# Kernel optimization log

Hardware: AMD Instinct MI355X
Metric: run time of the kernel (lower is better)

Reference implementation:

```python
import jax, jax.numpy as jnp
import numpy as np

B = 32          # num graphs
N = 4096        # nodes per graph (temporal length after reshape)
TOT = B * N     # 131072 total nodes
F = 64          # num_features
HS = 128        # hidden_dim_s
RS = 32         # rank_s
HT = 128        # hidden_dim_t
RT = 32         # rank_t
E = 1048576     # num edges


def setup_inputs() -> dict:
    key = jax.random.key(0)
    ks = jax.random.split(key, 20)
    x = jax.random.normal(ks[0], (TOT, F), jnp.float32)
    edge_index = jax.random.randint(ks[1], (2, E), 0, TOT, dtype=jnp.int64)
    batch = jnp.repeat(jnp.arange(B, dtype=jnp.int64), N)

    def lin(k, fan_in, fan_out):
        s = 1.0 / np.sqrt(fan_in)
        return jax.random.uniform(k, (fan_in, fan_out), jnp.float32, -s, s)

    def conv(k, cout, cin):
        s = 1.0 / np.sqrt(cin * 3)
        return jax.random.uniform(k, (cout, cin, 3), jnp.float32, -s, s)

    return {
        "x": x, "edge_index": edge_index, "batch": batch,
        "W1": lin(ks[2], F, HS), "b1": jnp.zeros((HS,), jnp.float32),
        "W2": lin(ks[3], HS, RS), "b2": jnp.zeros((RS,), jnp.float32),
        "W3": lin(ks[4], RS, HS), "b3": jnp.zeros((HS,), jnp.float32),
        "tW1": conv(ks[5], HT, HS), "tb1": jnp.zeros((HT,), jnp.float32),
        "tW2": conv(ks[6], RT, HT), "tb2": jnp.zeros((RT,), jnp.float32),
        "tW3": conv(ks[7], HT, RT), "tb3": jnp.zeros((HT,), jnp.float32),
        "Wpi": lin(ks[8], HT, 1), "bpi": jnp.zeros((1,), jnp.float32),
        "Wn": lin(ks[9], HT, 1), "bn": jnp.zeros((1,), jnp.float32),
        "Wp": lin(ks[10], HT, 1), "bp": jnp.zeros((1,), jnp.float32),
    }


def reference(x, edge_index, batch,
              W1, b1, W2, b2, W3, b3,
              tW1, tb1, tW2, tb2, tW3, tb3,
              Wpi, bpi, Wn, bn, Wp, bp):
    src, dst = edge_index[0], edge_index[1]
    n = x.shape[0]

    # GCN symmetric normalization with added self-loops (PyG GCNConv default)
    deg = jnp.zeros((n,), x.dtype).at[dst].add(1.0) + 1.0  # +1 self-loop
    dinv = jax.lax.rsqrt(deg)
    enorm = dinv[src] * dinv[dst]       # [E] edge normalization
    snorm = dinv * dinv                 # [n] self-loop normalization

    def gcn(h, W, b):
        h = h @ W                                            # [n, out]
        agg = jnp.zeros_like(h).at[dst].add(h[src] * enorm[:, None])
        return agg + h * snorm[:, None] + b

    xs = jax.nn.relu(gcn(x, W1, b1))
    xs = jax.nn.relu(gcn(xs, W2, b2))
    xs = jax.nn.relu(gcn(xs, W3, b3))    # [TOT, HS]

    num_graphs = B  # == batch.max() + 1 (batch is repeat(arange(B), N))
    xs = xs.reshape(num_graphs, -1, xs.shape[-1]).transpose(0, 2, 1)  # [B, HS, N]

    def conv1d(z, w, bias):
        y = jax.lax.conv_general_dilated(
            z, w, window_strides=(1,), padding=((1, 1),),
            dimension_numbers=("NCH", "OIH", "NCH"))
        return y + bias[None, :, None]

    xt = jax.nn.relu(conv1d(xs, tW1, tb1))
    xt = jax.nn.relu(conv1d(xt, tW2, tb2))
    xt = jax.nn.relu(conv1d(xt, tW3, tb3))                   # [B, HT, N]

    xt = xt.transpose(0, 2, 1).reshape(-1, xt.shape[1])      # [TOT, HT]

    pi = jax.nn.sigmoid(xt @ Wpi + bpi)
    nb = jax.nn.softplus(xt @ Wn + bn)
    p = jax.nn.sigmoid(xt @ Wp + bp)
    return (pi, nb, p)
```

## Files before the change

### kernel.cpp

```cpp
#include <hip/hip_runtime.h>
#include <cmath>

constexpr int TOT = 131072;
constexpr int NE  = 1048576;
constexpr int NMASK = 4095;

constexpr int NB   = 512;
constexpr int DPB  = 256;
constexpr int BCAP = 4096;
constexpr int EPB  = 8192;

typedef __attribute__((ext_vector_type(8))) short bf16x8;
typedef __attribute__((ext_vector_type(4))) float f32x4;

__device__ inline float bf2f(unsigned int u16) {
    union { unsigned int i; float f; } x; x.i = u16 << 16; return x.f;
}
__device__ inline unsigned short f2bf(float f) {
    union { float f; unsigned int i; } x; x.f = f;
    unsigned int r = (x.i + 0x7fffu + ((x.i >> 16) & 1u)) >> 16;
    return (unsigned short)r;
}
__device__ inline void unpack8(uint4 v, float* f) {
    f[0] = bf2f(v.x & 0xffffu); f[1] = bf2f(v.x >> 16);
    f[2] = bf2f(v.y & 0xffffu); f[3] = bf2f(v.y >> 16);
    f[4] = bf2f(v.z & 0xffffu); f[5] = bf2f(v.z >> 16);
    f[6] = bf2f(v.w & 0xffffu); f[7] = bf2f(v.w >> 16);
}
__device__ inline uint4 pack8(const float* f) {
    uint4 v;
    v.x = (unsigned)f2bf(f[0]) | ((unsigned)f2bf(f[1]) << 16);
    v.y = (unsigned)f2bf(f[2]) | ((unsigned)f2bf(f[3]) << 16);
    v.z = (unsigned)f2bf(f[4]) | ((unsigned)f2bf(f[5]) << 16);
    v.w = (unsigned)f2bf(f[6]) | ((unsigned)f2bf(f[7]) << 16);
    return v;
}

__global__ __launch_bounds__(256) void k_part(const int* __restrict__ src,
                                              const int* __restrict__ dst,
                                              int* __restrict__ gcur,
                                              unsigned* __restrict__ buf) {
    __shared__ int hist[NB];
    __shared__ int cbase[NB];
    __shared__ int lcur[NB];
    const int tid = threadIdx.x;
    const int e0 = blockIdx.x * EPB;

    for (int b = tid; b < NB; b += 256) hist[b] = 0;
    __syncthreads();
    for (int i = tid; i < EPB; i += 256)
        atomicAdd(&hist[dst[e0 + i] >> 8], 1);
    __syncthreads();
    for (int b = tid; b < NB; b += 256) {
        int c = hist[b];
        cbase[b] = (c > 0) ? atomicAdd(&gcur[b * 32], c) : 0;
        lcur[b] = 0;
    }
    __syncthreads();
    for (int i = tid; i < EPB; i += 256) {
        int e = e0 + i;
        int d = dst[e];
        int b = d >> 8;
        int p = atomicAdd(&lcur[b], 1);
        buf[b * BCAP + cbase[b] + p] = ((unsigned)src[e] << 8) | (unsigned)(d & 255);
    }
}

__global__ __launch_bounds__(256) void k_bcsr(const unsigned* __restrict__ buf,
                                              const int* __restrict__ gcur,
                                              int* __restrict__ adj,
                                              int2* __restrict__ rse,
                                              float* __restrict__ dinv) {
    __shared__ int cnt[DPB];
    __shared__ int start[DPB];
    __shared__ int cur[DPB];
    __shared__ int sc[DPB];
    const int b = blockIdx.x;
    const int tid = threadIdx.x;
    cnt[tid] = 0;
    __syncthreads();
    const int n = gcur[b * 32];
    const unsigned* eb = buf + b * BCAP;
    for (int i = tid; i < n; i += 256)
        atomicAdd(&cnt[eb[i] & 255u], 1);
    __syncthreads();
    int v = cnt[tid];
    sc[tid] = v;
    __syncthreads();
    for (int off = 1; off < 256; off <<= 1) {
        int a = sc[tid];
        int p = (tid >= off) ? sc[tid - off] : 0;
        __syncthreads();
        sc[tid] = a + p;
        __syncthreads();
    }
    int st = sc[tid] - v;
    start[tid] = st;
    cur[tid] = 0;
    int d = (b << 8) + tid;
    rse[d] = make_int2(b * BCAP + st, v);
    dinv[d] = rsqrtf((float)v + 1.0f);
    __syncthreads();
    for (int i = tid; i < n; i += 256) {
        unsigned w = eb[i];
        int dl = (int)(w & 255u);
        int p = atomicAdd(&cur[dl], 1);
        adj[b * BCAP + start[dl] + p] = (int)(w >> 8);
    }
}

__global__ __launch_bounds__(256) void k_packall(
    const float* __restrict__ W1, const float* __restrict__ W2, const float* __restrict__ W3,
    const float* __restrict__ tW1, const float* __restrict__ tW2, const float* __restrict__ tW3,
    unsigned short* __restrict__ g1, unsigned short* __restrict__ g2, unsigned short* __restrict__ g3,
    unsigned short* __restrict__ c1, unsigned short* __restrict__ c2, unsigned short* __restrict__ c3) {
    int gid = blockIdx.x * 256 + threadIdx.x;
    const float* w; unsigned short* wp; int CIN, COUT, taps, idx;
    if      (gid <  8192) { w = W1;  wp = g1; CIN = 64;  COUT = 128; taps = 1; idx = gid; }
    else if (gid < 12288) { w = W2;  wp = g2; CIN = 128; COUT = 32;  taps = 1; idx = gid - 8192; }
    else if (gid < 16384) { w = W3;  wp = g3; CIN = 32;  COUT = 128; taps = 1; idx = gid - 12288; }
    else if (gid < 65536) { w = tW1; wp = c1; CIN = 128; COUT = 128; taps = 3; idx = gid - 16384; }
    else if (gid < 77824) { w = tW2; wp = c2; CIN = 128; COUT = 32;  taps = 3; idx = gid - 65536; }
    else if (gid < 90112) { w = tW3; wp = c3; CIN = 32;  COUT = 128; taps = 3; idx = gid - 77824; }
    else return;
    int j = idx & 7;
    int L = (idx >> 3) & 63;
    int f = idx >> 9;
    int NT = COUT >> 4;
    int kc = f / NT, nt = f - kc * NT;
    int k = kc * 32 + (L >> 4) * 8 + j;
    int n = nt * 16 + (L & 15);
    float v;
    if (taps == 1) v = w[k * COUT + n];
    else { int t = k / CIN, c = k - t * CIN; v = w[(n * CIN + c) * 3 + t]; }
    wp[idx] = f2bf(v);
}

__global__ __launch_bounds__(256) void k_scale64b(const float4* __restrict__ x,
                                                  const float* __restrict__ dinv,
                                                  uint4* __restrict__ out) {
    int t = blockIdx.x * 256 + threadIdx.x;
    int row = t >> 3;
    float d = dinv[row];
    float4 v0 = x[t * 2], v1 = x[t * 2 + 1];
    float f[8] = { v0.x * d, v0.y * d, v0.z * d, v0.w * d,
                   v1.x * d, v1.y * d, v1.z * d, v1.w * d };
    out[t] = pack8(f);
}

template<int LC, int EPI>
__global__ __launch_bounds__(256) void k_gcsr(const uint4* __restrict__ xs,
                                              const int* __restrict__ adj,
                                              const int2* __restrict__ rse,
                                              const float* __restrict__ dinv,
                                              const float* __restrict__ bias,
                                              uint4* __restrict__ out) {
    int t = blockIdx.x * 256 + threadIdx.x;
    int d = t >> LC;
    int g = t & ((1 << LC) - 1);
    float a[8];
    unpack8(xs[t], a);
    int2 se = rse[d];
    int e = se.x, end = se.x + se.y;
    for (; e + 4 <= end; e += 4) {
        int s0 = adj[e], s1 = adj[e + 1], s2 = adj[e + 2], s3 = adj[e + 3];
        uint4 v0 = xs[(s0 << LC) + g];
        uint4 v1 = xs[(s1 << LC) + g];
        uint4 v2 = xs[(s2 << LC) + g];
        uint4 v3 = xs[(s3 << LC) + g];
        float f[8];
        unpack8(v0, f);
#pragma unroll
        for (int j = 0; j < 8; ++j) a[j] += f[j];
        unpack8(v1, f);
#pragma unroll
        for (int j = 0; j < 8; ++j) a[j] += f[j];
        unpack8(v2, f);
#pragma unroll
        for (int j = 0; j < 8; ++j) a[j] += f[j];
        unpack8(v3, f);
#pragma unroll
        for (int j = 0; j < 8; ++j) a[j] += f[j];
    }
    for (; e < end; ++e) {
        float f[8];
        unpack8(xs[(adj[e] << LC) + g], f);
#pragma unroll
        for (int j = 0; j < 8; ++j) a[j] += f[j];
    }
    float dv = dinv[d];
    if (EPI == 1) {
#pragma unroll
        for (int j = 0; j < 8; ++j)
            a[j] = fmaxf(fmaf(a[j], dv, bias[g * 8 + j]), 0.0f) * dv;
    } else {
#pragma unroll
        for (int j = 0; j < 8; ++j) a[j] *= dv;
    }
    out[t] = pack8(a);
}

template<int CIN, int COUT, int TAPS, bool RELU, bool BIAS, bool SOUT>
__global__ __launch_bounds__(256) void k_mm(const unsigned short* __restrict__ x,
                                            const bf16x8* __restrict__ wp,
                                            const float* __restrict__ bias,
                                            const float* __restrict__ dinv,
                                            unsigned short* __restrict__ y) {
    constexpr int ROWS = 64;
    constexpr int HALO = (TAPS == 3) ? 1 : 0;
    constexpr int TR = ROWS + 2 * HALO;
    constexpr int SC = CIN + 8;
    constexpr int NCH = CIN / 32;
    constexpr int NK = TAPS * NCH;
    constexpr int NT = COUT / 16;
    constexpr int WN = (COUT == 128) ? 2 : 1;
    constexpr int WM = (COUT == 128) ? 4 : 2;
    __shared__ __attribute__((aligned(16))) unsigned short tile[TR * SC];

    const int R0 = blockIdx.x * ROWS;
    const int n0 = R0 & NMASK; (void)n0;

    constexpr int NLD = TR * (CIN / 8);
    for (int idx = threadIdx.x; idx < NLD; idx += 256) {
        int tr = idx / (CIN / 8);
        int c8 = idx - tr * (CIN / 8);
        int ro = tr - HALO;
        bool valid = true;
        if (TAPS == 3) {
            if (ro < 0) valid = (n0 > 0);
            else if (ro >= ROWS) valid = (n0 + ROWS < 4096);
        }
        uint4 v = make_uint4(0, 0, 0, 0);
        if (valid) v = *(const uint4*)(x + (long)(R0 + ro) * CIN + c8 * 8);
        *(uint4*)(tile + tr * SC + c8 * 8) = v;
    }
    __syncthreads();

    const int lane = threadIdx.x & 63;
    const int w = threadIdx.x >> 6;
    const int l16 = lane & 15;
    const int q = lane >> 4;
    const int colbase = (COUT == 128) ? w * 32 : (w & 1) * 16;
    const int rowbase = (COUT == 128) ? 0 : (w >> 1) * 32;
    const int nt0 = colbase >> 4;

    f32x4 acc[WM][WN];
#pragma unroll
    for (int wm = 0; wm < WM; ++wm)
#pragma unroll
        for (int nt = 0; nt < WN; ++nt) acc[wm][nt] = (f32x4){0.f, 0.f, 0.f, 0.f};

    const bf16x8* __restrict__ wpl = wp + lane;

#pragma unroll
    for (int kc = 0; kc < NK; ++kc) {
        const int tap = (TAPS == 3) ? (kc / NCH) : 0;
        const int ch  = (TAPS == 3) ? (kc - tap * NCH) : kc;
        bf16x8 a[WM];
#pragma unroll
        for (int wm = 0; wm < WM; ++wm)
            a[wm] = *(const bf16x8*)(tile + (rowbase + wm * 16 + l16 + tap) * SC + ch * 32 + q * 8);
        bf16x8 b[WN];
#pragma unroll
        for (int nt = 0; nt < WN; ++nt)
            b[nt] = wpl[(kc * NT + nt0 + nt) * 64];
#pragma unroll
        for (int wm = 0; wm < WM; ++wm)
#pragma unroll
            for (int nt = 0; nt < WN; ++nt)
                acc[wm][nt] = __builtin_amdgcn_mfma_f32_16x16x32_bf16(a[wm], b[nt], acc[wm][nt], 0, 0, 0);
    }

#pragma unroll
    for (int wm = 0; wm < WM; ++wm) {
#pragma unroll
        for (int nt = 0; nt < WN; ++nt) {
            int col = colbase + nt * 16 + l16;
            float bi = BIAS ? bias[col] : 0.0f;
#pragma unroll
            for (int r = 0; r < 4; ++r) {
                int row = R0 + rowbase + wm * 16 + q * 4 + r;
                float v = acc[wm][nt][r] + bi;
                if (RELU) v = fmaxf(v, 0.0f);
                if (SOUT) v *= dinv[row];
                y[(long)row * COUT + col] = f2bf(v);
            }
        }
    }
}

__global__ __launch_bounds__(256) void k_conv_heads(
    const unsigned short* __restrict__ x, const bf16x8* __restrict__ wp,
    const float* __restrict__ bias,
    const float* __restrict__ Wpi, const float* __restrict__ bpi,
    const float* __restrict__ Wn,  const float* __restrict__ bn,
    const float* __restrict__ Wp,  const float* __restrict__ bp,
    float* __restrict__ out) {
    constexpr int CIN = 32;
    constexpr int ROWS = 64, HALO = 1, TR = 66, SC = CIN + 8;
    constexpr int NK = 3, NT = 8, WN = 2, WM = 4;
    __shared__ __attribute__((aligned(16))) unsigned short tile[TR * SC];
    __shared__ unsigned short xts[64 * 130];

    const int R0 = blockIdx.x * ROWS;
    const int n0 = R0 & NMASK;

    constexpr int NLD = TR * (CIN / 8);
    for (int idx = threadIdx.x; idx < NLD; idx += 256) {
        int tr = idx / (CIN / 8);
        int c8 = idx - tr * (CIN / 8);
        int ro = tr - HALO;
        bool valid = true;
        if (ro < 0) valid = (n0 > 0);
        else if (ro >= ROWS) valid = (n0 + ROWS < 4096);
        uint4 v = make_uint4(0, 0, 0, 0);
        if (valid) v = *(const uint4*)(x + (long)(R0 + ro) * CIN + c8 * 8);
        *(uint4*)(tile + tr * SC + c8 * 8) = v;
    }
    __syncthreads();

    const int lane = threadIdx.x & 63;
    const int w = threadIdx.x >> 6;
    const int l16 = lane & 15;
    const int q = lane >> 4;
    const int colbase = w * 32;
    const int nt0 = colbase >> 4;

    f32x4 acc[WM][WN];
#pragma unroll
    for (int wm = 0; wm < WM; ++wm)
#pragma unroll
        for (int nt = 0; nt < WN; ++nt) acc[wm][nt] = (f32x4){0.f, 0.f, 0.f, 0.f};

    const bf16x8* __restrict__ wpl = wp + lane;

#pragma unroll
    for (int kc = 0; kc < NK; ++kc) {
        bf16x8 a[WM];
#pragma unroll
        for (int wm = 0; wm < WM; ++wm)
            a[wm] = *(const bf16x8*)(tile + (wm * 16 + l16 + kc) * SC + q * 8);
        bf16x8 b[WN];
#pragma unroll
        for (int nt = 0; nt < WN; ++nt)
            b[nt] = wpl[(kc * NT + nt0 + nt) * 64];
#pragma unroll
        for (int wm = 0; wm < WM; ++wm)
#pragma unroll
            for (int nt = 0; nt < WN; ++nt)
                acc[wm][nt] = __builtin_amdgcn_mfma_f32_16x16x32_bf16(a[wm], b[nt], acc[wm][nt], 0, 0, 0);
    }

#pragma unroll
    for (int wm = 0; wm < WM; ++wm) {
#pragma unroll
        for (int nt = 0; nt < WN; ++nt) {
            int col = colbase + nt * 16 + l16;
            float bi = bias[col];
#pragma unroll
            for (int r = 0; r < 4; ++r) {
                int row = wm * 16 + q * 4 + r;
                xts[row * 130 + col] = f2bf(fmaxf(acc[wm][nt][r] + bi, 0.0f));
            }
        }
    }
    __syncthreads();
    if (threadIdx.x < 192) {
        int h = threadIdx.x >> 6;
        int row = threadIdx.x & 63;
        const float* Wh = (h == 0) ? Wpi : (h == 1) ? Wn : Wp;
        float s = 0.0f;
        const unsigned short* xr = xts + row * 130;
#pragma unroll
        for (int c2 = 0; c2 < 64; ++c2) {
            unsigned u = *(const unsigned*)(xr + c2 * 2);
            s = fmaf(bf2f(u & 0xffffu), Wh[c2 * 2], s);
            s = fmaf(bf2f(u >> 16), Wh[c2 * 2 + 1], s);
        }
        float bb = (h == 0) ? bpi[0] : (h == 1) ? bn[0] : bp[0];
        float z = s + bb;
        float o;
        if (h == 1) o = (z > 20.0f) ? z : log1pf(expf(z));
        else        o = 1.0f / (1.0f + expf(-z));
        out[h * TOT + R0 + row] = o;
    }
}

extern "C" void kernel_launch(void* const* d_in, const int* in_sizes, int n_in,
                              void* d_out, int out_size, void* d_ws, size_t ws_size,
                              hipStream_t stream) {
    const float* x   = (const float*)d_in[0];
    const int*   ei  = (const int*)d_in[1];
    const int*   src = ei;
    const int*   dst = ei + NE;
    const float* W1 = (const float*)d_in[3];
    const float* b1 = (const float*)d_in[4];
    const float* W2 = (const float*)d_in[5];
    const float* b2 = (const float*)d_in[6];
    const float* W3 = (const float*)d_in[7];
    const float* b3 = (const float*)d_in[8];
    const float* tW1 = (const float*)d_in[9];
    const float* tb1 = (const float*)d_in[10];
    const float* tW2 = (const float*)d_in[11];
    const float* tb2 = (const float*)d_in[12];
    const float* tW3 = (const float*)d_in[13];
    const float* tb3 = (const float*)d_in[14];
    const float* Wpi = (const float*)d_in[15];
    const float* bpi = (const float*)d_in[16];
    const float* Wn  = (const float*)d_in[17];
    const float* bn  = (const float*)d_in[18];
    const float* Wp  = (const float*)d_in[19];
    const float* bp  = (const float*)d_in[20];

    char* ws = (char*)d_ws;
    float* dinv = (float*)(ws + (0ull << 20));
    int*   gcur = (int*)  (ws + (1ull << 20));
    int2*  rse  = (int2*) (ws + (1ull << 20) + (256 << 10));
    unsigned short* wpG1 = (unsigned short*)(ws + (3ull << 20));
    unsigned short* wpG2 = (unsigned short*)(ws + (3ull << 20) + (128 << 10));
    unsigned short* wpG3 = (unsigned short*)(ws + (3ull << 20) + (256 << 10));
    unsigned short* wpC1 = (unsigned short*)(ws + (3ull << 20) + (384 << 10));
    unsigned short* wpC2 = (unsigned short*)(ws + (3ull << 20) + (512 << 10));
    unsigned short* wpC3 = (unsigned short*)(ws + (3ull << 20) + (640 << 10));
    unsigned* buf = (unsigned*)(ws + (4ull << 20));
    int* adj = (int*)(ws + (12ull << 20));
    unsigned short* Xa = (unsigned short*)(ws + (24ull  << 20));
    unsigned short* Xb = (unsigned short*)(ws + (44ull  << 20));
    unsigned short* Xc = (unsigned short*)(ws + (80ull  << 20));
    unsigned short* Xd = (unsigned short*)(ws + (116ull << 20));
    unsigned short* Xe = (unsigned short*)(ws + (128ull << 20));

    hipMemsetAsync(gcur, 0, NB * 32 * sizeof(int), stream);
    k_packall<<<352, 256, 0, stream>>>(W1, W2, W3, tW1, tW2, tW3,
                                       wpG1, wpG2, wpG3, wpC1, wpC2, wpC3);

    k_part<<<NE / EPB, 256, 0, stream>>>(src, dst, gcur, buf);
    k_bcsr<<<NB, 256, 0, stream>>>(buf, gcur, adj, rse, dinv);

    k_scale64b<<<TOT * 8 / 256, 256, 0, stream>>>((const float4*)x, dinv, (uint4*)Xa);
    k_gcsr<3, 2><<<TOT * 8 / 256, 256, 0, stream>>>((const uint4*)Xa, adj, rse, dinv,
                                                    nullptr, (uint4*)Xb);
    k_mm<64, 128, 1, true, true, false>
        <<<TOT / 64, 256, 0, stream>>>(Xb, (const bf16x8*)wpG1, b1, dinv, Xc);

    k_mm<128, 32, 1, false, false, true>
        <<<TOT / 64, 256, 0, stream>>>(Xc, (const bf16x8*)wpG2, nullptr, dinv, Xd);
    k_gcsr<2, 1><<<TOT * 4 / 256, 256, 0, stream>>>((const uint4*)Xd, adj, rse, dinv,
                                                    b2, (uint4*)Xe);

    k_gcsr<2, 2><<<TOT * 4 / 256, 256, 0, stream>>>((const uint4*)Xe, adj, rse, dinv,
                                                    nullptr, (uint4*)Xd);
    k_mm<32, 128, 1, true, true, false>
        <<<TOT / 64, 256, 0, stream>>>(Xd, (const bf16x8*)wpG3, b3, dinv, Xb);

    k_mm<128, 128, 3, true, true, false>
        <<<TOT / 64, 256, 0, stream>>>(Xb, (const bf16x8*)wpC1, tb1, nullptr, Xc);
    k_mm<128, 32, 3, true, true, false>
        <<<TOT / 64, 256, 0, stream>>>(Xc, (const bf16x8*)wpC2, tb2, nullptr, Xd);

    k_conv_heads<<<TOT / 64, 256, 0, stream>>>(Xd, (const bf16x8*)wpC3, tb3,
                                               Wpi, bpi, Wn, bn, Wp, bp, (float*)d_out);
}
```

Before: 301.4 us.

## Fuse GCN neighbor aggregation into the following matmul kernel

Adds a k_gmm kernel that gathers CSR neighbor rows, scales by dinv, writes the aggregated tile to shared memory and runs the MFMA matmul with bias and ReLU in the same launch. It replaces the separate gather and matmul kernels for GCN layers 1 and 3, so the intermediate aggregated activations no longer round-trip through global memory and two launches are removed. Edges per partition block shrink from 8192 to 2048, which launches more partition blocks. The cost is that each block does the irregular gather before the MFMA phase, with four threads per row and less parallelism in the gather.

Result: faster. 286.7 us (-4.9%).

```diff
diff --git a/kernel.cpp b/kernel.cpp
--- a/kernel.cpp
+++ b/kernel.cpp
@@ -8,7 +8,7 @@
 constexpr int NB   = 512;
 constexpr int DPB  = 256;
 constexpr int BCAP = 4096;
-constexpr int EPB  = 8192;
+constexpr int EPB  = 2048;
 
 typedef __attribute__((ext_vector_type(8))) short bf16x8;
 typedef __attribute__((ext_vector_type(4))) float f32x4;
@@ -148,7 +148,7 @@
     out[t] = pack8(f);
 }
 
-template<int LC, int EPI>
+template<int LC>
 __global__ __launch_bounds__(256) void k_gcsr(const uint4* __restrict__ xs,
                                               const int* __restrict__ adj,
                                               const int2* __restrict__ rse,
@@ -189,15 +189,123 @@
         for (int j = 0; j < 8; ++j) a[j] += f[j];
     }
     float dv = dinv[d];
-    if (EPI == 1) {
-#pragma unroll
-        for (int j = 0; j < 8; ++j)
-            a[j] = fmaxf(fmaf(a[j], dv, bias[g * 8 + j]), 0.0f) * dv;
-    } else {
-#pragma unroll
-        for (int j = 0; j < 8; ++j) a[j] *= dv;
-    }
+#pragma unroll
+    for (int j = 0; j < 8; ++j)
+        a[j] = fmaxf(fmaf(a[j], dv, bias[g * 8 + j]), 0.0f) * dv;
     out[t] = pack8(a);
+}
+
+template<int CIN, bool RELU>
+__global__ __launch_bounds__(256) void k_gmm(const uint4* __restrict__ xs,
+                                             const int* __restrict__ adj,
+                                             const int2* __restrict__ rse,
+                                             const float* __restrict__ dinv,
+                                             const bf16x8* __restrict__ wp,
+                                             const float* __restrict__ bias,
+                                             unsigned short* __restrict__ y) {
+    constexpr int COUT = 128;
+    constexpr int ROWS = 64;
+    constexpr int SC = CIN + 8;
+    constexpr int NV = CIN / 8;
+    constexpr int VPT = NV / 4;
+    constexpr int NK = CIN / 32;
+    constexpr int NT = COUT / 16;
+    constexpr int WN = 2, WM = 4;
+    __shared__ __attribute__((aligned(16))) unsigned short tile[ROWS * SC];
+
+    const int R0 = blockIdx.x * ROWS;
+    const int tid = threadIdx.x;
+
+    {
+        int r = R0 + (tid >> 2);
+        int g = tid & 3;
+        const uint4* base = xs + (long)r * NV + g * VPT;
+        float a[VPT * 8];
+#pragma unroll
+        for (int v = 0; v < VPT; ++v) unpack8(base[v], a + v * 8);
+        int2 se = rse[r];
+        int e = se.x, end = se.x + se.y;
+        for (; e + 2 <= end; e += 2) {
+            int s0 = adj[e], s1 = adj[e + 1];
+            const uint4* p0 = xs + (long)s0 * NV + g * VPT;
+            const uint4* p1 = xs + (long)s1 * NV + g * VPT;
+            uint4 v0[VPT], v1[VPT];
+#pragma unroll
+            for (int v = 0; v < VPT; ++v) { v0[v] = p0[v]; v1[v] = p1[v]; }
+            float f[VPT * 8];
+#pragma unroll
+            for (int v = 0; v < VPT; ++v) unpack8(v0[v], f + v * 8);
+#pragma unroll
+            for (int j = 0; j < VPT * 8; ++j) a[j] += f[j];
+#pragma unroll
+            for (int v = 0; v < VPT; ++v) unpack8(v1[v], f + v * 8);
+#pragma unroll
+            for (int j = 0; j < VPT * 8; ++j) a[j] += f[j];
+        }
+        for (; e < end; ++e) {
+            const uint4* p0 = xs + (long)adj[e] * NV + g * VPT;
+            float f[VPT * 8];
+#pragma unroll
+            for (int v = 0; v < VPT; ++v) unpack8(p0[v], f + v * 8);
+#pragma unroll
+            for (int j = 0; j < VPT * 8; ++j) a[j] += f[j];
+        }
+        float dv = dinv[r];
+#pragma unroll
+        for (int j = 0; j < VPT * 8; ++j) a[j] *= dv;
+        uint4* dst4 = (uint4*)(tile + (tid >> 2) * SC + g * VPT * 8);
+#pragma unroll
+        for (int v = 0; v < VPT; ++v) dst4[v] = pack8(a + v * 8);
+    }
+    __syncthreads();
+
+    const int lane = threadIdx.x & 63;
+    const int w = threadIdx.x >> 6;
+    const int l16 = lane & 15;
+    const int q = lane >> 4;
+    const int colbase = w * 32;
+    const int nt0 = colbase >> 4;
+
+    f32x4 acc[WM][WN];
+#pragma unroll
+    for (int wm = 0; wm < WM; ++wm)
+#pragma unroll
+        for (int nt = 0; nt < WN; ++nt) acc[wm][nt] = (f32x4){0.f, 0.f, 0.f, 0.f};
+
+    const bf16x8* __restrict__ wpl = wp + lane;
+
+#pragma unroll
+    for (int kc = 0; kc < NK; ++kc) {
+        bf16x8 a[WM];
+#pragma unroll
+        for (int wm = 0; wm < WM; ++wm)
+            a[wm] = *(const bf16x8*)(tile + (wm * 16 + l16) * SC + kc * 32 + q * 8);
+        bf16x8 b[WN];
+#pragma unroll
+        for (int nt = 0; nt < WN; ++nt)
+            b[nt] = wpl[(kc * NT + nt0 + nt) * 64];
+#pragma unroll
+        for (int wm = 0; wm < WM; ++wm)
+#pragma unroll
+            for (int nt = 0; nt < WN; ++nt)
+                acc[wm][nt] = __builtin_amdgcn_mfma_f32_16x16x32_bf16(a[wm], b[nt], acc[wm][nt], 0, 0, 0);
+    }
+
+#pragma unroll
+    for (int wm = 0; wm < WM; ++wm) {
+#pragma unroll
+        for (int nt = 0; nt < WN; ++nt) {
+            int col = colbase + nt * 16 + l16;
+            float bi = bias[col];
+#pragma unroll
+            for (int r = 0; r < 4; ++r) {
+                int row = R0 + wm * 16 + q * 4 + r;
+                float v = acc[wm][nt][r] + bi;
+                if (RELU) v = fmaxf(v, 0.0f);
+                y[(long)row * COUT + col] = f2bf(v);
+            }
+        }
+    }
 }
 
 template<int CIN, int COUT, int TAPS, bool RELU, bool BIAS, bool SOUT>
@@ -438,20 +546,16 @@
     k_bcsr<<<NB, 256, 0, stream>>>(buf, gcur, adj, rse, dinv);
 
     k_scale64b<<<TOT * 8 / 256, 256, 0, stream>>>((const float4*)x, dinv, (uint4*)Xa);
-    k_gcsr<3, 2><<<TOT * 8 / 256, 256, 0, stream>>>((const uint4*)Xa, adj, rse, dinv,
-                                                    nullptr, (uint4*)Xb);
-    k_mm<64, 128, 1, true, true, false>
-        <<<TOT / 64, 256, 0, stream>>>(Xb, (const bf16x8*)wpG1, b1, dinv, Xc);
+    k_gmm<64, true><<<TOT / 64, 256, 0, stream>>>((const uint4*)Xa, adj, rse, dinv,
+                                                  (const bf16x8*)wpG1, b1, Xc);
 
     k_mm<128, 32, 1, false, false, true>
         <<<TOT / 64, 256, 0, stream>>>(Xc, (const bf16x8*)wpG2, nullptr, dinv, Xd);
-    k_gcsr<2, 1><<<TOT * 4 / 256, 256, 0, stream>>>((const uint4*)Xd, adj, rse, dinv,
-                                                    b2, (uint4*)Xe);
-
-    k_gcsr<2, 2><<<TOT * 4 / 256, 256, 0, stream>>>((const uint4*)Xe, adj, rse, dinv,
-                                                    nullptr, (uint4*)Xd);
-    k_mm<32, 128, 1, true, true, false>
-        <<<TOT / 64, 256, 0, stream>>>(Xd, (const bf16x8*)wpG3, b3, dinv, Xb);
+    k_gcsr<2><<<TOT * 4 / 256, 256, 0, stream>>>((const uint4*)Xd, adj, rse, dinv,
+                                                 b2, (uint4*)Xe);
+
+    k_gmm<32, true><<<TOT / 64, 256, 0, stream>>>((const uint4*)Xe, adj, rse, dinv,
+                                                  (const bf16x8*)wpG3, b3, Xb);
 
     k_mm<128, 128, 3, true, true, false>
         <<<TOT / 64, 256, 0, stream>>>(Xb, (const bf16x8*)wpC1, tb1, nullptr, Xc);
```
